# Kernel optimization log

Measured on AMD Instinct MI355X. Metric: run time of the kernel, lower is better.

## Reference

```python
import jax, jax.numpy as jnp
import numpy as np

K = 512  # codebook size


def setup_inputs() -> dict:
    key = jax.random.key(0)
    k1, k2 = jax.random.split(key)
    z_e = jax.random.normal(k1, (16, 4096, 64), dtype=jnp.float32)
    codebook = jax.random.normal(k2, (K, 64), dtype=jnp.float32)
    return {"z_e": z_e, "codebook": codebook}


def reference(z_e, codebook):
    # squared euclidean distances (..., K): ||z||^2 - 2 z.c + ||c||^2
    z_sq = jnp.sum(z_e * z_e, axis=-1, keepdims=True)            # (B,T,1)
    c_sq = jnp.sum(codebook * codebook, axis=-1)                  # (K,)
    cross = jnp.einsum('btd,kd->btk', z_e, codebook)              # (B,T,K)
    distances = z_sq - 2.0 * cross + c_sq                         # (B,T,K)
    q_z_x = jnp.argmin(distances, axis=-1).astype(jnp.int32)      # (B,T)
    e_k = codebook[q_z_x]                                         # (B,T,D)
    # straight-through estimator
    z_q = z_e + jax.lax.stop_gradient(e_k - z_e)
    # perplexity of code usage
    idx = q_z_x.reshape(-1)
    n = idx.shape[0]
    counts = jnp.zeros((K,), dtype=z_e.dtype).at[idx].add(1.0)
    avg_probs = counts / n
    perplexity = jnp.exp(-jnp.sum(avg_probs * jnp.log(avg_probs + 1e-10)))
    return z_q, q_z_x, e_k, perplexity
```

## Files before the change

### kernel.cpp

```cpp
#include <hip/hip_runtime.h>
#include <math.h>

#define NTOK (16 * 4096)
#define DIM  64
#define KC   512
#define TPB  64

__global__ __launch_bounds__(256, 4)
void vq_main(const float* __restrict__ z_e, const float* __restrict__ cb,
             float* __restrict__ z_q, float* __restrict__ qzx,
             float* __restrict__ e_k, int* __restrict__ counts)
{
    __shared__ float zs[TPB][DIM + 1];
    __shared__ float csq[KC];
    __shared__ float dred[4][TPB];
    __shared__ int   kred[4][TPB];
    __shared__ int   hist[KC];

    const int tid = threadIdx.x;
    const long tok0 = (long)blockIdx.x * TPB;

    hist[tid] = 0;
    hist[tid + 256] = 0;

    {
        const float4* zg = (const float4*)(z_e + tok0 * DIM);
        #pragma unroll
        for (int it = 0; it < 4; ++it) {
            const int f4 = it * 256 + tid;
            const float4 v = zg[f4];
            const int row = f4 >> 4;
            const int c4  = (f4 & 15) << 2;
            zs[row][c4 + 0] = v.x; zs[row][c4 + 1] = v.y;
            zs[row][c4 + 2] = v.z; zs[row][c4 + 3] = v.w;
        }
    }

    #pragma unroll
    for (int it = 0; it < 2; ++it) {
        const int k = it * 256 + tid;
        const float4* cr = (const float4*)(cb + (size_t)k * DIM);
        float a0 = 0.f, a1 = 0.f, a2 = 0.f, a3 = 0.f;
        #pragma unroll
        for (int j = 0; j < 4; ++j) {
            const float4 v0 = cr[j], v1 = cr[4 + j], v2 = cr[8 + j], v3 = cr[12 + j];
            a0 += v0.x * v0.x + v0.y * v0.y + v0.z * v0.z + v0.w * v0.w;
            a1 += v1.x * v1.x + v1.y * v1.y + v1.z * v1.z + v1.w * v1.w;
            a2 += v2.x * v2.x + v2.y * v2.y + v2.z * v2.z + v2.w * v2.w;
            a3 += v3.x * v3.x + v3.y * v3.y + v3.z * v3.z + v3.w * v3.w;
        }
        csq[k] = (a0 + a1) + (a2 + a3);
    }
    __syncthreads();

    const int lane = tid & 63;
    float z[DIM];
    #pragma unroll
    for (int d = 0; d < DIM; ++d) z[d] = zs[lane][d];

    float s0 = 0.f, s1 = 0.f, s2 = 0.f, s3 = 0.f;
    #pragma unroll
    for (int d = 0; d < 16; ++d) {
        s0 += z[d]      * z[d];
        s1 += z[16 + d] * z[16 + d];
        s2 += z[32 + d] * z[32 + d];
        s3 += z[48 + d] * z[48 + d];
    }
    const float zsq = (s0 + s1) + (s2 + s3);

    const int wvu = __builtin_amdgcn_readfirstlane(tid >> 6);
    const int kbase = wvu * 128;

    float dmin = INFINITY;
    int   kmin = 0;
    #pragma unroll 2
    for (int kk = 0; kk < 128; ++kk) {
        const int k = kbase + kk;
        const float4* c4p = (const float4*)(cb + (size_t)k * DIM);
        float a0 = 0.f, a1 = 0.f, a2 = 0.f, a3 = 0.f;
        #pragma unroll
        for (int j = 0; j < 4; ++j) {
            const float4 c0 = c4p[j], c1 = c4p[4 + j], c2 = c4p[8 + j], c3 = c4p[12 + j];
            a0 = fmaf(z[4 * j + 0], c0.x, a0);
            a0 = fmaf(z[4 * j + 1], c0.y, a0);
            a0 = fmaf(z[4 * j + 2], c0.z, a0);
            a0 = fmaf(z[4 * j + 3], c0.w, a0);
            a1 = fmaf(z[16 + 4 * j + 0], c1.x, a1);
            a1 = fmaf(z[16 + 4 * j + 1], c1.y, a1);
            a1 = fmaf(z[16 + 4 * j + 2], c1.z, a1);
            a1 = fmaf(z[16 + 4 * j + 3], c1.w, a1);
            a2 = fmaf(z[32 + 4 * j + 0], c2.x, a2);
            a2 = fmaf(z[32 + 4 * j + 1], c2.y, a2);
            a2 = fmaf(z[32 + 4 * j + 2], c2.z, a2);
            a2 = fmaf(z[32 + 4 * j + 3], c2.w, a2);
            a3 = fmaf(z[48 + 4 * j + 0], c3.x, a3);
            a3 = fmaf(z[48 + 4 * j + 1], c3.y, a3);
            a3 = fmaf(z[48 + 4 * j + 2], c3.z, a3);
            a3 = fmaf(z[48 + 4 * j + 3], c3.w, a3);
        }
        const float dot  = (a0 + a1) + (a2 + a3);
        const float dist = (zsq - 2.0f * dot) + csq[k];
        if (dist < dmin) { dmin = dist; kmin = k; }
    }

    dred[tid >> 6][lane] = dmin;
    kred[tid >> 6][lane] = kmin;
    __syncthreads();

    if (tid < 64) {
        float dm = dred[0][tid];
        int   km = kred[0][tid];
        #pragma unroll
        for (int j = 1; j < 4; ++j) {
            const float dj = dred[j][tid];
            const int   kj = kred[j][tid];
            if (dj < dm) { dm = dj; km = kj; }
        }
        kred[0][tid] = km;
        atomicAdd(&hist[km], 1);
        qzx[tok0 + tid] = (float)km;
    }
    __syncthreads();

    atomicAdd(&counts[tid],       hist[tid]);
    atomicAdd(&counts[tid + 256], hist[tid + 256]);

    {
        float4* eo = (float4*)(e_k + tok0 * DIM);
        float4* zo = (float4*)(z_q + tok0 * DIM);
        #pragma unroll
        for (int it = 0; it < 4; ++it) {
            const int f4  = it * 256 + tid;
            const int row = f4 >> 4;
            const int c4  = (f4 & 15) << 2;
            const int km  = kred[0][row];
            const float4 cv = ((const float4*)(cb + (size_t)km * DIM))[f4 & 15];
            float4 zv;
            zv.x = zs[row][c4 + 0]; zv.y = zs[row][c4 + 1];
            zv.z = zs[row][c4 + 2]; zv.w = zs[row][c4 + 3];
            float4 q;
            q.x = zv.x + (cv.x - zv.x);
            q.y = zv.y + (cv.y - zv.y);
            q.z = zv.z + (cv.z - zv.z);
            q.w = zv.w + (cv.w - zv.w);
            eo[f4] = cv;
            zo[f4] = q;
        }
    }
}

__global__ void vq_perp(const int* __restrict__ counts, float* __restrict__ perp)
{
    const int tid = threadIdx.x;
    const float p = (float)counts[tid] * (1.0f / 65536.0f);
    float s = p * logf(p + 1e-10f);
    #pragma unroll
    for (int off = 32; off > 0; off >>= 1) s += __shfl_down(s, off);
    __shared__ float red[8];
    if ((tid & 63) == 0) red[tid >> 6] = s;
    __syncthreads();
    if (tid == 0) {
        float tot = 0.f;
        #pragma unroll
        for (int j = 0; j < 8; ++j) tot += red[j];
        perp[0] = expf(-tot);
    }
}

extern "C" void kernel_launch(void* const* d_in, const int* in_sizes, int n_in,
                              void* d_out, int out_size, void* d_ws, size_t ws_size,
                              hipStream_t stream)
{
    const float* z_e = (const float*)d_in[0];
    const float* cb  = (const float*)d_in[1];

    float* out  = (float*)d_out;
    float* z_q  = out;
    float* qzx  = out + (size_t)NTOK * DIM;
    float* e_k  = qzx + NTOK;
    float* perp = e_k + (size_t)NTOK * DIM;

    int* counts = (int*)d_ws;

    hipMemsetAsync(counts, 0, KC * sizeof(int), stream);
    vq_main<<<NTOK / TPB, 256, 0, stream>>>(z_e, cb, z_q, qzx, e_k, counts);
    vq_perp<<<1, KC, 0, stream>>>(counts, perp);
}
```

Before: 193.6 us.

## Use split-fp16 MFMA distance pass with exact fp32 candidate refinement

Replaces the scalar fp32 dot-product search with an MFMA-based pass that splits z and the codebook into high and low fp16 parts to approximate fp32 distances. Each token keeps up to 7 candidates within a margin of the best, or falls back to a full search when ambiguous. A second kernel recomputes exact fp32 distances for only those candidates. The aim is to move the dominant distance cost onto matrix cores, at the price of extra launches, a workspace round trip, and possible warp divergence from the fallback path.

```diff
diff --git a/kernel.cpp b/kernel.cpp
--- a/kernel.cpp
+++ b/kernel.cpp
@@ -1,30 +1,158 @@
 #include <hip/hip_runtime.h>
 #include <math.h>
 
-#define NTOK (16 * 4096)
+#define NTOK 65536
 #define DIM  64
 #define KC   512
-#define TPB  64
-
-__global__ __launch_bounds__(256, 4)
-void vq_main(const float* __restrict__ z_e, const float* __restrict__ cb,
-             float* __restrict__ z_q, float* __restrict__ qzx,
-             float* __restrict__ e_k, int* __restrict__ counts)
-{
-    __shared__ float zs[TPB][DIM + 1];
-    __shared__ float csq[KC];
-    __shared__ float dred[4][TPB];
-    __shared__ int   kred[4][TPB];
+#define EPS  0.0625f
+
+typedef _Float16 half8 __attribute__((ext_vector_type(8)));
+typedef float    f32x16 __attribute__((ext_vector_type(16)));
+
+#define WS_COUNTS 0
+#define WS_CSQ    2048
+#define WS_BPK    4096
+#define WS_CANDS  135168
+
+__global__ void vq_prep(const float* __restrict__ cb, _Float16* __restrict__ Bpk,
+                        float* __restrict__ csqg)
+{
+    const int k = blockIdx.x, d = threadIdx.x;
+    const float c = cb[k * 64 + d];
+    const _Float16 hh = (_Float16)c;
+    const _Float16 ll = (_Float16)(c - (float)hh);
+    Bpk[k * 128 + d]      = hh;
+    Bpk[k * 128 + 64 + d] = ll;
+    float p = c * c;
+    #pragma unroll
+    for (int off = 32; off > 0; off >>= 1) p += __shfl_down(p, off);
+    if (d == 0) csqg[k] = p;
+}
+
+__global__ void vq_dist(const float* __restrict__ z_e, const _Float16* __restrict__ Bpk,
+                        const float* __restrict__ csqg, short* __restrict__ candsg)
+{
+    __shared__ int cnt[128];
+    __shared__ int flg[128];
+    __shared__ __align__(16) short krec[128][8];
+
+    const int tid = threadIdx.x;
+    if (tid < 128) { cnt[tid] = 0; flg[tid] = 0; }
+    __syncthreads();
+
+    const int l = tid & 63, w = tid >> 6;
+    const int col = l & 31, h = l >> 5;
+    const long t = (long)blockIdx.x * 128 + w * 32 + col;
+
+    half8 azh[4], azl[4];
+    #pragma unroll
+    for (int c = 0; c < 4; ++c) {
+        const float* zp = z_e + t * 64 + c * 16 + h * 8;
+        const float4 u0 = *(const float4*)zp;
+        const float4 u1 = *(const float4*)(zp + 4);
+        const float vv[8] = {u0.x, u0.y, u0.z, u0.w, u1.x, u1.y, u1.z, u1.w};
+        half8 zh, zl;
+        #pragma unroll
+        for (int i = 0; i < 8; ++i) {
+            const _Float16 hh = (_Float16)vv[i];
+            zh[i] = hh;
+            zl[i] = (_Float16)(vv[i] - (float)hh);
+        }
+        azh[c] = zh; azl[c] = zl;
+    }
+
+    float b1[16], b2[16];
+    int   k1[16];
+    #pragma unroll
+    for (int j = 0; j < 16; ++j) { b1[j] = INFINITY; b2[j] = INFINITY; k1[j] = 0; }
+
+    f32x16 zerov;
+    #pragma unroll
+    for (int j = 0; j < 16; ++j) zerov[j] = 0.0f;
+
+    const _Float16* bbase = Bpk + (size_t)col * 128 + h * 8;
+
+    for (int nt = 0; nt < 16; ++nt) {
+        const int n0 = nt * 32;
+        const _Float16* bp = bbase + (size_t)n0 * 128;
+        half8 bch[4], bcl[4];
+        #pragma unroll
+        for (int c = 0; c < 4; ++c) {
+            bch[c] = *(const half8*)(bp + c * 16);
+            bcl[c] = *(const half8*)(bp + 64 + c * 16);
+        }
+        const float csql = csqg[n0 + col];
+
+        f32x16 acc = __builtin_amdgcn_mfma_f32_32x32x16_f16(azh[0], bch[0], zerov, 0, 0, 0);
+        #pragma unroll
+        for (int c = 1; c < 4; ++c)
+            acc = __builtin_amdgcn_mfma_f32_32x32x16_f16(azh[c], bch[c], acc, 0, 0, 0);
+        #pragma unroll
+        for (int c = 0; c < 4; ++c)
+            acc = __builtin_amdgcn_mfma_f32_32x32x16_f16(azl[c], bch[c], acc, 0, 0, 0);
+        #pragma unroll
+        for (int c = 0; c < 4; ++c)
+            acc = __builtin_amdgcn_mfma_f32_32x32x16_f16(azh[c], bcl[c], acc, 0, 0, 0);
+
+        const int kk = n0 + col;
+        #pragma unroll
+        for (int j = 0; j < 16; ++j) {
+            const float d = fmaf(acc[j], -2.0f, csql);
+            const bool lt = d < b1[j];
+            b2[j] = lt ? b1[j] : fminf(b2[j], d);
+            k1[j] = lt ? kk : k1[j];
+            b1[j] = lt ? d : b1[j];
+        }
+    }
+
+    #pragma unroll
+    for (int j = 0; j < 16; ++j) {
+        float d = b1[j];
+        int   k = k1[j];
+        #pragma unroll
+        for (int m = 1; m <= 16; m <<= 1) {
+            const float od = __shfl_xor(d, m);
+            const int   ok = __shfl_xor(k, m);
+            const bool bet = (od < d) || (od == d && ok < k);
+            d = bet ? od : d;
+            k = bet ? ok : k;
+        }
+        const int tokl = w * 32 + (j & 3) + 8 * (j >> 2) + 4 * h;
+        if (b1[j] < d + EPS) {
+            const int idx = atomicAdd(&cnt[tokl], 1);
+            if (idx < 7) krec[tokl][1 + idx] = (short)k1[j];
+            else flg[tokl] = 1;
+        }
+        if (b2[j] < d + EPS) flg[tokl] = 1;
+    }
+    __syncthreads();
+
+    if (tid < 128) {
+        const int c = cnt[tid];
+        const bool f = (flg[tid] != 0) || (c > 7);
+        krec[tid][0] = f ? (short)0x7FFF : (short)c;
+        const long tok = (long)blockIdx.x * 128 + tid;
+        ((int4*)candsg)[tok] = *(int4*)&krec[tid][0];
+    }
+}
+
+__global__ void vq_refine(const float* __restrict__ z_e, const float* __restrict__ cb,
+                          const short* __restrict__ candsg,
+                          float* __restrict__ z_q, float* __restrict__ qzx,
+                          float* __restrict__ e_k, int* __restrict__ counts)
+{
+    __shared__ float zs[64][65];
+    __shared__ int   kwin[64];
     __shared__ int   hist[KC];
 
     const int tid = threadIdx.x;
-    const long tok0 = (long)blockIdx.x * TPB;
+    const long tok0 = (long)blockIdx.x * 64;
 
     hist[tid] = 0;
     hist[tid + 256] = 0;
 
     {
-        const float4* zg = (const float4*)(z_e + tok0 * DIM);
+        const float4* zg = (const float4*)(z_e + tok0 * 64);
         #pragma unroll
         for (int it = 0; it < 4; ++it) {
             const int f4 = it * 256 + tid;
@@ -35,90 +163,52 @@
             zs[row][c4 + 2] = v.z; zs[row][c4 + 3] = v.w;
         }
     }
-
-    #pragma unroll
-    for (int it = 0; it < 2; ++it) {
-        const int k = it * 256 + tid;
-        const float4* cr = (const float4*)(cb + (size_t)k * DIM);
-        float a0 = 0.f, a1 = 0.f, a2 = 0.f, a3 = 0.f;
+    __syncthreads();
+
+    const int g = tid >> 2, sub = tid & 3;
+
+    float s = 0.f;
+    #pragma unroll
+    for (int d = 0; d < 16; ++d) { const float zv = zs[g][16 * sub + d]; s += zv * zv; }
+    const float spair = s + __shfl_xor(s, 1);
+    const float zsq   = spair + __shfl_xor(spair, 2);
+
+    const int4 rc = ((const int4*)candsg)[tok0 + g];
+    const short* rp = (const short*)&rc;
+    const int cw = rp[0];
+    const int nc = (cw == 0x7FFF) ? KC : cw;
+
+    float dm = INFINITY;
+    int   km = 0;
+    for (int i = 0; i < nc; ++i) {
+        const int k = (cw == 0x7FFF) ? i : (int)rp[1 + i];
+        const float4* cf = (const float4*)(cb + (size_t)k * 64 + 16 * sub);
+        float a = 0.f, q = 0.f;
         #pragma unroll
         for (int j = 0; j < 4; ++j) {
-            const float4 v0 = cr[j], v1 = cr[4 + j], v2 = cr[8 + j], v3 = cr[12 + j];
-            a0 += v0.x * v0.x + v0.y * v0.y + v0.z * v0.z + v0.w * v0.w;
-            a1 += v1.x * v1.x + v1.y * v1.y + v1.z * v1.z + v1.w * v1.w;
-            a2 += v2.x * v2.x + v2.y * v2.y + v2.z * v2.z + v2.w * v2.w;
-            a3 += v3.x * v3.x + v3.y * v3.y + v3.z * v3.z + v3.w * v3.w;
-        }
-        csq[k] = (a0 + a1) + (a2 + a3);
-    }
-    __syncthreads();
-
-    const int lane = tid & 63;
-    float z[DIM];
-    #pragma unroll
-    for (int d = 0; d < DIM; ++d) z[d] = zs[lane][d];
-
-    float s0 = 0.f, s1 = 0.f, s2 = 0.f, s3 = 0.f;
-    #pragma unroll
-    for (int d = 0; d < 16; ++d) {
-        s0 += z[d]      * z[d];
-        s1 += z[16 + d] * z[16 + d];
-        s2 += z[32 + d] * z[32 + d];
-        s3 += z[48 + d] * z[48 + d];
-    }
-    const float zsq = (s0 + s1) + (s2 + s3);
-
-    const int wvu = __builtin_amdgcn_readfirstlane(tid >> 6);
-    const int kbase = wvu * 128;
-
-    float dmin = INFINITY;
-    int   kmin = 0;
-    #pragma unroll 2
-    for (int kk = 0; kk < 128; ++kk) {
-        const int k = kbase + kk;
-        const float4* c4p = (const float4*)(cb + (size_t)k * DIM);
-        float a0 = 0.f, a1 = 0.f, a2 = 0.f, a3 = 0.f;
-        #pragma unroll
-        for (int j = 0; j < 4; ++j) {
-            const float4 c0 = c4p[j], c1 = c4p[4 + j], c2 = c4p[8 + j], c3 = c4p[12 + j];
-            a0 = fmaf(z[4 * j + 0], c0.x, a0);
-            a0 = fmaf(z[4 * j + 1], c0.y, a0);
-            a0 = fmaf(z[4 * j + 2], c0.z, a0);
-            a0 = fmaf(z[4 * j + 3], c0.w, a0);
-            a1 = fmaf(z[16 + 4 * j + 0], c1.x, a1);
-            a1 = fmaf(z[16 + 4 * j + 1], c1.y, a1);
-            a1 = fmaf(z[16 + 4 * j + 2], c1.z, a1);
-            a1 = fmaf(z[16 + 4 * j + 3], c1.w, a1);
-            a2 = fmaf(z[32 + 4 * j + 0], c2.x, a2);
-            a2 = fmaf(z[32 + 4 * j + 1], c2.y, a2);
-            a2 = fmaf(z[32 + 4 * j + 2], c2.z, a2);
-            a2 = fmaf(z[32 + 4 * j + 3], c2.w, a2);
-            a3 = fmaf(z[48 + 4 * j + 0], c3.x, a3);
-            a3 = fmaf(z[48 + 4 * j + 1], c3.y, a3);
-            a3 = fmaf(z[48 + 4 * j + 2], c3.z, a3);
-            a3 = fmaf(z[48 + 4 * j + 3], c3.w, a3);
-        }
-        const float dot  = (a0 + a1) + (a2 + a3);
-        const float dist = (zsq - 2.0f * dot) + csq[k];
-        if (dist < dmin) { dmin = dist; kmin = k; }
-    }
-
-    dred[tid >> 6][lane] = dmin;
-    kred[tid >> 6][lane] = kmin;
+            const float4 v = cf[j];
+            a = fmaf(zs[g][16 * sub + 4 * j + 0], v.x, a);
+            a = fmaf(zs[g][16 * sub + 4 * j + 1], v.y, a);
+            a = fmaf(zs[g][16 * sub + 4 * j + 2], v.z, a);
+            a = fmaf(zs[g][16 * sub + 4 * j + 3], v.w, a);
+            q += v.x * v.x + v.y * v.y + v.z * v.z + v.w * v.w;
+        }
+        const float ap  = a + __shfl_xor(a, 1);
+        const float dot = ap + __shfl_xor(ap, 2);
+        const float qp  = q + __shfl_xor(q, 1);
+        const float csq = qp + __shfl_xor(qp, 2);
+        const float dist = (zsq - 2.0f * dot) + csq;
+        const bool bet = (dist < dm) || (dist == dm && k < km);
+        dm = bet ? dist : dm;
+        km = bet ? k : km;
+    }
+    if (sub == 0) kwin[g] = km;
     __syncthreads();
 
     if (tid < 64) {
-        float dm = dred[0][tid];
-        int   km = kred[0][tid];
-        #pragma unroll
-        for (int j = 1; j < 4; ++j) {
-            const float dj = dred[j][tid];
-            const int   kj = kred[j][tid];
-            if (dj < dm) { dm = dj; km = kj; }
-        }
-        kred[0][tid] = km;
-        atomicAdd(&hist[km], 1);
-        qzx[tok0 + tid] = (float)km;
+        const int k2 = kwin[tid];
+        atomicAdd(&hist[k2], 1);
+        qzx[tok0 + tid] = (float)k2;
     }
     __syncthreads();
 
@@ -126,25 +216,25 @@
     atomicAdd(&counts[tid + 256], hist[tid + 256]);
 
     {
-        float4* eo = (float4*)(e_k + tok0 * DIM);
-        float4* zo = (float4*)(z_q + tok0 * DIM);
+        float4* eo = (float4*)(e_k + tok0 * 64);
+        float4* zo = (float4*)(z_q + tok0 * 64);
         #pragma unroll
         for (int it = 0; it < 4; ++it) {
             const int f4  = it * 256 + tid;
             const int row = f4 >> 4;
             const int c4  = (f4 & 15) << 2;
-            const int km  = kred[0][row];
-            const float4 cv = ((const float4*)(cb + (size_t)km * DIM))[f4 & 15];
+            const int kmr = kwin[row];
+            const float4 cv = ((const float4*)(cb + (size_t)kmr * 64))[f4 & 15];
             float4 zv;
             zv.x = zs[row][c4 + 0]; zv.y = zs[row][c4 + 1];
             zv.z = zs[row][c4 + 2]; zv.w = zs[row][c4 + 3];
-            float4 q;
-            q.x = zv.x + (cv.x - zv.x);
-            q.y = zv.y + (cv.y - zv.y);
-            q.z = zv.z + (cv.z - zv.z);
-            q.w = zv.w + (cv.w - zv.w);
+            float4 qq;
+            qq.x = zv.x + (cv.x - zv.x);
+            qq.y = zv.y + (cv.y - zv.y);
+            qq.z = zv.z + (cv.z - zv.z);
+            qq.w = zv.w + (cv.w - zv.w);
             eo[f4] = cv;
-            zo[f4] = q;
+            zo[f4] = qq;
         }
     }
 }
@@ -180,9 +270,15 @@
     float* e_k  = qzx + NTOK;
     float* perp = e_k + (size_t)NTOK * DIM;
 
-    int* counts = (int*)d_ws;
+    char* ws = (char*)d_ws;
+    int*      counts = (int*)(ws + WS_COUNTS);
+    float*    csqg   = (float*)(ws + WS_CSQ);
+    _Float16* Bpk    = (_Float16*)(ws + WS_BPK);
+    short*    cands  = (short*)(ws + WS_CANDS);
 
     hipMemsetAsync(counts, 0, KC * sizeof(int), stream);
-    vq_main<<<NTOK / TPB, 256, 0, stream>>>(z_e, cb, z_q, qzx, e_k, counts);
+    vq_prep<<<KC, 64, 0, stream>>>(cb, Bpk, csqg);
+    vq_dist<<<NTOK / 128, 256, 0, stream>>>(z_e, Bpk, csqg, cands);
+    vq_refine<<<NTOK / 64, 256, 0, stream>>>(z_e, cb, cands, z_q, qzx, e_k, counts);
     vq_perp<<<1, KC, 0, stream>>>(counts, perp);
 }
```

New measurement: 350.6 us. +81.1%, slower.
